# Kernel optimization log

Measured on AMD Instinct MI355X. Metric: run time of the kernel, lower is better.

## Reference

```python
import jax, jax.numpy as jnp
import numpy as np

N_PTS = 500000
R = 8            # channels per plane (num_channels=24 // 3)
FEAT = 24        # concat of 3 planes
HID = 168        # mlp_dim
OUT = 35
SIZES = [128, 256, 512]  # plane resolutions per level (plane_size=512, level_factor=0.5)
XYZ_MIN, XYZ_MAX = -2.0, 2.0


def setup_inputs() -> dict:
    key = jax.random.key(0)
    ks = jax.random.split(key, 64)
    inp = {"xyz": jax.random.uniform(ks[0], (N_PTS, 3), dtype=jnp.float32)}
    ki = 1
    for i, s in enumerate(SIZES):
        # planes stored [R, H, W]; torch init randn*0.1
        inp[f"xy{i}"] = jax.random.normal(ks[ki + 0], (R, s, s), dtype=jnp.float32) * 0.1
        inp[f"xz{i}"] = jax.random.normal(ks[ki + 1], (R, s, s), dtype=jnp.float32) * 0.1
        inp[f"yz{i}"] = jax.random.normal(ks[ki + 2], (R, s, s), dtype=jnp.float32) * 0.1
        inp[f"w1_{i}"] = jax.random.normal(ks[ki + 3], (FEAT, HID), dtype=jnp.float32) * 0.05
        inp[f"b1_{i}"] = jnp.zeros((HID,), jnp.float32)
        inp[f"w2_{i}"] = jax.random.normal(ks[ki + 4], (HID, HID), dtype=jnp.float32) * 0.05
        inp[f"b2_{i}"] = jnp.zeros((HID,), jnp.float32)
        inp[f"w3_{i}"] = jax.random.normal(ks[ki + 5], (HID, OUT), dtype=jnp.float32) * 0.05
        inp[f"b3_{i}"] = jnp.zeros((OUT,), jnp.float32)
        ki += 6
    return inp


def _bilinear(plane, gx, gy):
    # plane: [C,H,W]; gx in [-1,1] maps to W, gy maps to H; align_corners=True
    C, H, W = plane.shape
    ix = (gx + 1.0) * 0.5 * (W - 1)
    iy = (gy + 1.0) * 0.5 * (H - 1)
    x0 = jnp.floor(ix).astype(jnp.int32)
    y0 = jnp.floor(iy).astype(jnp.int32)
    wx = ix - x0
    wy = iy - y0
    x0c = jnp.clip(x0, 0, W - 1); x1c = jnp.clip(x0 + 1, 0, W - 1)
    y0c = jnp.clip(y0, 0, H - 1); y1c = jnp.clip(y0 + 1, 0, H - 1)
    v00 = plane[:, y0c, x0c]  # [C,N]
    v01 = plane[:, y0c, x1c]
    v10 = plane[:, y1c, x0c]
    v11 = plane[:, y1c, x1c]
    top = v00 * (1 - wx) + v01 * wx
    bot = v10 * (1 - wx) + v11 * wx
    return (top * (1 - wy) + bot * wy).T  # [N,C]


def _forward(xyz, planes, mlps):
    nrm = (xyz - XYZ_MIN) / (XYZ_MAX - XYZ_MIN) * 2.0 - 1.0  # [N,3]
    nx, ny, nz = nrm[:, 0], nrm[:, 1], nrm[:, 2]
    tmp = 0.0
    for (xy, xz, yz), (w1, b1, w2, b2, w3, b3) in zip(planes, mlps):
        # xy_plane[H=X,W=Y] sampled with grid (gx=ny, gy=nx), etc.
        feat = jnp.concatenate([
            _bilinear(xy, ny, nx),
            _bilinear(xz, nz, nx),
            _bilinear(yz, nz, ny),
        ], axis=-1)  # [N,24]
        h = jax.nn.relu(feat @ w1 + b1)
        h = jax.nn.relu(h @ w2 + b2)
        tmp = tmp + (h @ w3 + b3)
    # inference head: features[:27], rotations[27:31] raw; scale sigmoid; opacity*10
    return jnp.concatenate([tmp[:, :31], jax.nn.sigmoid(tmp[:, 31:34]), tmp[:, 34:] * 10.0], axis=-1)


def reference(xyz, xy0, xz0, yz0, w1_0, b1_0, w2_0, b2_0, w3_0, b3_0,
              xy1, xz1, yz1, w1_1, b1_1, w2_1, b2_1, w3_1, b3_1,
              xy2, xz2, yz2, w1_2, b1_2, w2_2, b2_2, w3_2, b3_2):
    planes = [(xy0, xz0, yz0), (xy1, xz1, yz1), (xy2, xz2, yz2)]
    mlps = [(w1_0, b1_0, w2_0, b2_0, w3_0, b3_0),
            (w1_1, b1_1, w2_1, b2_1, w3_1, b3_1),
            (w1_2, b1_2, w2_2, b2_2, w3_2, b3_2)]
    return _forward(xyz, planes, mlps)
```

## Files before the change

### kernel.cpp

```cpp
#include <hip/hip_runtime.h>

#define N_PTS 500000
#define FEAT 24
#define HID 168
#define OUT_C 35
#define MT 64
#define H_STR 176
#define WREG (32 * H_STR + 16)

#define WF1_OFF 0
#define WF2_OFF 18432
#define WF3_OFF 129024
#define W_TOTAL 156672
#define PL_S0 (W_TOTAL)
#define PL_S1 (PL_S0 + 393216)
#define PL_S2 (PL_S1 + 1572864)

#define PREP_W_BLOCKS 612

typedef short bf16x8 __attribute__((ext_vector_type(8)));
typedef float f32x4 __attribute__((ext_vector_type(4)));

__device__ __forceinline__ unsigned short f2bf(float f) {
    union { float f; unsigned int u; } v; v.f = f;
    unsigned int u = v.u;
    return (unsigned short)((u + 0x7FFFu + ((u >> 16) & 1u)) >> 16);
}
__device__ __forceinline__ float bf2f(unsigned short h) {
    union { unsigned int u; float f; } v; v.u = ((unsigned int)h) << 16;
    return v.f;
}
__device__ __forceinline__ unsigned int pk_bf16(float a, float b) {
    unsigned int r;
    asm("v_cvt_pk_bf16_f32 %0, %1, %2" : "=v"(r) : "v"(a), "v"(b));
    return r;
}
__device__ __forceinline__ f32x4 mfma16(bf16x8 a, bf16x8 b, f32x4 c) {
    return __builtin_amdgcn_mfma_f32_16x16x32_bf16(a, b, c, 0, 0, 0);
}

__global__ __launch_bounds__(256) void prep_all(
    const float* __restrict__ xy0, const float* __restrict__ xz0, const float* __restrict__ yz0,
    const float* __restrict__ xy1, const float* __restrict__ xz1, const float* __restrict__ yz1,
    const float* __restrict__ xy2, const float* __restrict__ xz2, const float* __restrict__ yz2,
    const float* __restrict__ w1a, const float* __restrict__ w2a, const float* __restrict__ w3a,
    const float* __restrict__ w1b, const float* __restrict__ w2b, const float* __restrict__ w3b,
    const float* __restrict__ w1c, const float* __restrict__ w2c, const float* __restrict__ w3c,
    const float* __restrict__ b1a, const float* __restrict__ b2a, const float* __restrict__ b3a,
    const float* __restrict__ b1b, const float* __restrict__ b2b, const float* __restrict__ b3b,
    const float* __restrict__ b1c, const float* __restrict__ b2c, const float* __restrict__ b3c,
    unsigned short* __restrict__ ws)
{
    if (blockIdx.x < PREP_W_BLOCKS) {
        int id = blockIdx.x * 256 + threadIdx.x;
        const float* w1[3] = {w1a, w1b, w1c};
        const float* w2[3] = {w2a, w2b, w2c};
        const float* w3[3] = {w3a, w3b, w3c};
        const float* b1[3] = {b1a, b1b, b1c};
        const float* b2[3] = {b2a, b2b, b2c};
        const float* b3[3] = {b3a, b3b, b3c};
        float v = 0.f;
        if (id < WF2_OFF) {
            int s = id / 6144, r = id % 6144;
            int mt = r >> 9, q = r & 511, lane = q >> 3, j = q & 7;
            int n = mt * 16 + (lane & 15), k = (lane >> 4) * 8 + j;
            if (n < HID) {
                if (k < FEAT)       v = w1[s][k * HID + n];
                else if (k == FEAT) v = b1[s][n];
            }
        } else if (id < WF3_OFF) {
            int t = id - WF2_OFF;
            int s = t / 36864, r = t % 36864;
            int fi = r >> 9, q = r & 511, lane = q >> 3, j = q & 7;
            int kk = fi / 12, mt = fi % 12;
            int n = mt * 16 + (lane & 15), k = kk * 32 + (lane >> 4) * 8 + j;
            if (n < HID) {
                if (k < HID)        v = w2[s][k * HID + n];
                else if (k == HID)  v = b2[s][n];
            }
        } else {
            int t = id - WF3_OFF;
            int s = t / 9216, r = t % 9216;
            int fi = r >> 9, q = r & 511, lane = q >> 3, j = q & 7;
            int mt = fi / 6, kk = fi % 6;
            int n = mt * 16 + (lane & 15), k = kk * 32 + (lane >> 4) * 8 + j;
            if (n < OUT_C) {
                if (k < HID)        v = w3[s][k * OUT_C + n];
                else if (k == HID)  v = b3[s][n];
            }
        }
        ws[id] = f2bf(v);
        return;
    }

    const float* pls[9] = {xy0, xz0, yz0, xy1, xz1, yz1, xy2, xz2, yz2};
    int b = blockIdx.x - PREP_W_BLOCKS;
    int s, pl, chunk, SS, base;
    if (b < 192)        { s = 0; SS = 16384;  pl = b / 64;   chunk = b % 64;    base = PL_S0; }
    else if (b < 960)   { int t = b - 192; s = 1; SS = 65536;  pl = t / 256;  chunk = t % 256;  base = PL_S1; }
    else                { int t = b - 960; s = 2; SS = 262144; pl = t / 1024; chunk = t % 1024; base = PL_S2; }
    const float* src = pls[s * 3 + pl];
    int pos = chunk * 256 + threadIdx.x;
    uint4 pk;
    unsigned int* po = (unsigned int*)&pk;
    #pragma unroll
    for (int c = 0; c < 4; ++c) {
        float f0 = src[(2 * c)     * SS + pos];
        float f1 = src[(2 * c + 1) * SS + pos];
        po[c] = pk_bf16(f0, f1);
    }
    *reinterpret_cast<uint4*>(&ws[base + pl * SS * 8 + pos * 8]) = pk;
}

__global__ __launch_bounds__(128, 4) void tri_mlp(
    const float* __restrict__ xyz,
    const unsigned short* __restrict__ wpack,
    float* __restrict__ out)
{
    __shared__ __align__(16) unsigned short H[2 * WREG];

    const int tid  = threadIdx.x;
    const int wave = tid >> 6;
    const int lane = tid & 63;
    const int quad = lane >> 4;
    const int l16  = lane & 15;
    const int p0   = blockIdx.x * MT;
    const int prow = wave * 32;
    unsigned short* Hw = H + wave * WREG;

    if (lane < 32)
        *reinterpret_cast<uint4*>(&Hw[lane * H_STR + HID]) = make_uint4(0x3F80u, 0u, 0u, 0u);
    if (lane < 8) ((unsigned int*)(Hw + 32 * H_STR))[lane] = 0u;

    float X[2], Y[2], Z[2];
    #pragma unroll
    for (int ni = 0; ni < 2; ++ni) {
        int gp = min(p0 + prow + ni * 16 + l16, N_PTS - 1);
        X[ni] = xyz[gp * 3 + 0];
        Y[ni] = xyz[gp * 3 + 1];
        Z[ni] = xyz[gp * 3 + 2];
    }

    f32x4 c3[2][3];
    #pragma unroll
    for (int mt = 0; mt < 3; ++mt) {
        c3[0][mt] = (f32x4){0.f, 0.f, 0.f, 0.f};
        c3[1][mt] = (f32x4){0.f, 0.f, 0.f, 0.f};
    }

    #pragma unroll 1
    for (int s = 0; s < 3; ++s) {
        int S, sbase;
        if (s == 0)      { S = 128; sbase = PL_S0; }
        else if (s == 1) { S = 256; sbase = PL_S1; }
        else             { S = 512; sbase = PL_S2; }

        bf16x8 B1[2];
        #pragma unroll
        for (int ni = 0; ni < 2; ++ni) {
            uint4 pk = {0x3F80u, 0u, 0u, 0u};
            if (quad < 3) {
                float gx, gy;
                if (quad == 0)      { gx = Y[ni]; gy = X[ni]; }
                else if (quad == 1) { gx = Z[ni]; gy = X[ni]; }
                else                { gx = Z[ni]; gy = Y[ni]; }
                gx *= 0.5f; gy *= 0.5f;
                float ix = (gx + 1.0f) * 0.5f * (float)(S - 1);
                float iy = (gy + 1.0f) * 0.5f * (float)(S - 1);
                float fx = floorf(ix), fy = floorf(iy);
                int x0 = (int)fx, y0 = (int)fy;
                float wx = ix - fx, wy = iy - fy;
                int x0c = min(max(x0, 0), S - 1);
                int x1c = min(x0 + 1, S - 1);
                int y0c = min(max(y0, 0), S - 1);
                int y1c = min(y0 + 1, S - 1);
                const unsigned short* pcl = wpack + sbase + (quad << 3) * S * S;
                uint4 q00 = *(const uint4*)&pcl[(y0c * S + x0c) * 8];
                uint4 q01 = *(const uint4*)&pcl[(y0c * S + x1c) * 8];
                uint4 q10 = *(const uint4*)&pcl[(y1c * S + x0c) * 8];
                uint4 q11 = *(const uint4*)&pcl[(y1c * S + x1c) * 8];
                float w00 = (1.f - wx) * (1.f - wy), w01 = wx * (1.f - wy);
                float w10 = (1.f - wx) * wy,         w11 = wx * wy;
                const unsigned int* u00 = (const unsigned int*)&q00;
                const unsigned int* u01 = (const unsigned int*)&q01;
                const unsigned int* u10 = (const unsigned int*)&q10;
                const unsigned int* u11 = (const unsigned int*)&q11;
                unsigned int* po = (unsigned int*)&pk;
                #pragma unroll
                for (int h = 0; h < 4; ++h) {
                    float a0 = bf2f((unsigned short)(u00[h] & 0xFFFF)) * w00
                             + bf2f((unsigned short)(u01[h] & 0xFFFF)) * w01
                             + bf2f((unsigned short)(u10[h] & 0xFFFF)) * w10
                             + bf2f((unsigned short)(u11[h] & 0xFFFF)) * w11;
                    float a1 = bf2f((unsigned short)(u00[h] >> 16)) * w00
                             + bf2f((unsigned short)(u01[h] >> 16)) * w01
                             + bf2f((unsigned short)(u10[h] >> 16)) * w10
                             + bf2f((unsigned short)(u11[h] >> 16)) * w11;
                    po[h] = pk_bf16(a0, a1);
                }
            }
            B1[ni] = *reinterpret_cast<bf16x8*>(&pk);
        }

        {
            const unsigned short* w1f = wpack + WF1_OFF + s * 6144;
            #pragma unroll
            for (int mt = 0; mt < 11; ++mt) {
                bf16x8 a = *(const bf16x8*)&w1f[mt * 512 + lane * 8];
                #pragma unroll
                for (int ni = 0; ni < 2; ++ni) {
                    f32x4 c = mfma16(a, B1[ni], (f32x4){0.f, 0.f, 0.f, 0.f});
                    unsigned int u0 = pk_bf16(fmaxf(c[0], 0.f), fmaxf(c[1], 0.f));
                    unsigned int u1 = pk_bf16(fmaxf(c[2], 0.f), fmaxf(c[3], 0.f));
                    if (mt < 10 || quad < 2)
                        *reinterpret_cast<uint2*>(&Hw[(ni * 16 + l16) * H_STR + mt * 16 + quad * 4]) =
                            make_uint2(u0, u1);
                }
            }
        }

        bf16x8 B2[2][6];
        #pragma unroll
        for (int ni = 0; ni < 2; ++ni)
            #pragma unroll
            for (int kk = 0; kk < 6; ++kk)
                B2[ni][kk] = *(const bf16x8*)&Hw[(ni * 16 + l16) * H_STR + kk * 32 + quad * 8];

        {
            const unsigned short* w2f = wpack + WF2_OFF + s * 36864;
            #pragma unroll 1
            for (int mt = 0; mt < 11; ++mt) {
                f32x4 c20 = {0.f, 0.f, 0.f, 0.f};
                f32x4 c21 = c20;
                #pragma unroll
                for (int kk = 0; kk < 6; ++kk) {
                    bf16x8 a = *(const bf16x8*)&w2f[(kk * 12 + mt) * 512 + lane * 8];
                    c20 = mfma16(a, B2[0][kk], c20);
                    c21 = mfma16(a, B2[1][kk], c21);
                }
                if (mt < 10 || quad < 2) {
                    unsigned int u00 = pk_bf16(fmaxf(c20[0], 0.f), fmaxf(c20[1], 0.f));
                    unsigned int u01 = pk_bf16(fmaxf(c20[2], 0.f), fmaxf(c20[3], 0.f));
                    *reinterpret_cast<uint2*>(&Hw[(l16) * H_STR + mt * 16 + quad * 4]) =
                        make_uint2(u00, u01);
                    unsigned int u10 = pk_bf16(fmaxf(c21[0], 0.f), fmaxf(c21[1], 0.f));
                    unsigned int u11 = pk_bf16(fmaxf(c21[2], 0.f), fmaxf(c21[3], 0.f));
                    *reinterpret_cast<uint2*>(&Hw[(16 + l16) * H_STR + mt * 16 + quad * 4]) =
                        make_uint2(u10, u11);
                }
            }
        }

        {
            const unsigned short* w3f = wpack + WF3_OFF + s * 9216;
            #pragma unroll 1
            for (int kk = 0; kk < 6; ++kk) {
                bf16x8 b30 = *(const bf16x8*)&Hw[(l16) * H_STR + kk * 32 + quad * 8];
                bf16x8 b31 = *(const bf16x8*)&Hw[(16 + l16) * H_STR + kk * 32 + quad * 8];
                #pragma unroll
                for (int mt = 0; mt < 3; ++mt) {
                    bf16x8 a = *(const bf16x8*)&w3f[(mt * 6 + kk) * 512 + lane * 8];
                    c3[0][mt] = mfma16(a, b30, c3[0][mt]);
                    c3[1][mt] = mfma16(a, b31, c3[1][mt]);
                }
            }
        }
    }

    float* Hf = (float*)Hw;
    #pragma unroll
    for (int ni = 0; ni < 2; ++ni) {
        int row = ni * 16 + l16;
        #pragma unroll
        for (int mt = 0; mt < 3; ++mt) {
            #pragma unroll
            for (int r = 0; r < 4; ++r) {
                int ch = mt * 16 + quad * 4 + r;
                if (ch < OUT_C) {
                    float v = c3[ni][mt][r];
                    if (ch >= 31 && ch < 34)      v = 1.0f / (1.0f + expf(-v));
                    else if (ch == 34)            v *= 10.0f;
                    Hf[row * 35 + ch] = v;
                }
            }
        }
    }
    if (p0 + prow < N_PTS) {
        const int base = (p0 + prow) * 35;
        #pragma unroll
        for (int t = 0; t < 5; ++t) {
            int off = t * 256 + lane * 4;
            if (off < 1120) {
                f32x4 v = *(const f32x4*)&Hf[off];
                __builtin_nontemporal_store(v, reinterpret_cast<f32x4*>(&out[base + off]));
            }
        }
    }
}

extern "C" void kernel_launch(void* const* d_in, const int* in_sizes, int n_in,
                              void* d_out, int out_size, void* d_ws, size_t ws_size,
                              hipStream_t stream) {
    (void)in_sizes; (void)n_in; (void)out_size; (void)ws_size;
    const float* xyz  = (const float*)d_in[0];
    const float* xy0  = (const float*)d_in[1];
    const float* xz0  = (const float*)d_in[2];
    const float* yz0  = (const float*)d_in[3];
    const float* w1_0 = (const float*)d_in[4];
    const float* b1_0 = (const float*)d_in[5];
    const float* w2_0 = (const float*)d_in[6];
    const float* b2_0 = (const float*)d_in[7];
    const float* w3_0 = (const float*)d_in[8];
    const float* b3_0 = (const float*)d_in[9];
    const float* xy1  = (const float*)d_in[10];
    const float* xz1  = (const float*)d_in[11];
    const float* yz1  = (const float*)d_in[12];
    const float* w1_1 = (const float*)d_in[13];
    const float* b1_1 = (const float*)d_in[14];
    const float* w2_1 = (const float*)d_in[15];
    const float* b2_1 = (const float*)d_in[16];
    const float* w3_1 = (const float*)d_in[17];
    const float* b3_1 = (const float*)d_in[18];
    const float* xy2  = (const float*)d_in[19];
    const float* xz2  = (const float*)d_in[20];
    const float* yz2  = (const float*)d_in[21];
    const float* w1_2 = (const float*)d_in[22];
    const float* b1_2 = (const float*)d_in[23];
    const float* w2_2 = (const float*)d_in[24];
    const float* b2_2 = (const float*)d_in[25];
    const float* w3_2 = (const float*)d_in[26];
    const float* b3_2 = (const float*)d_in[27];

    unsigned short* ws = (unsigned short*)d_ws;
    float* out = (float*)d_out;

    prep_all<<<PREP_W_BLOCKS + 4032, 256, 0, stream>>>(
        xy0, xz0, yz0, xy1, xz1, yz1, xy2, xz2, yz2,
        w1_0, w2_0, w3_0, w1_1, w2_1, w3_1, w1_2, w2_2, w3_2,
        b1_0, b2_0, b3_0, b1_1, b2_1, b3_1, b1_2, b2_2, b3_2,
        ws);

    tri_mlp<<<(N_PTS + MT - 1) / MT, 128, 0, stream>>>(xyz, ws, out);
}
```

Baseline: 351.6 us.

## Halve points per wave to 16 and raise occupancy target

Each wave now handles one 16-point MFMA column tile instead of two, so the block tile drops from 64 to 32 points and the per-wave LDS region shrinks. Launch bounds go from 4 to 6 blocks per SM, aiming for more resident waves to hide the latency of the bilinear gathers. The trade-off is that each weight fragment loaded from global/L2 now feeds only one MFMA instead of two, which doubles weight traffic per point. The bounds clamp was removed because 500000 is divisible by 32.

```diff
diff --git a/kernel.cpp b/kernel.cpp
--- a/kernel.cpp
+++ b/kernel.cpp
@@ -4,9 +4,9 @@
 #define FEAT 24
 #define HID 168
 #define OUT_C 35
-#define MT 64
+#define MT 32
 #define H_STR 176
-#define WREG (32 * H_STR + 16)
+#define WREG (16 * H_STR + 16)
 
 #define WF1_OFF 0
 #define WF2_OFF 18432
@@ -112,7 +112,7 @@
     *reinterpret_cast<uint4*>(&ws[base + pl * SS * 8 + pos * 8]) = pk;
 }
 
-__global__ __launch_bounds__(128, 4) void tri_mlp(
+__global__ __launch_bounds__(128, 6) void tri_mlp(
     const float* __restrict__ xyz,
     const unsigned short* __restrict__ wpack,
     float* __restrict__ out)
@@ -125,28 +125,21 @@
     const int quad = lane >> 4;
     const int l16  = lane & 15;
     const int p0   = blockIdx.x * MT;
-    const int prow = wave * 32;
+    const int prow = wave * 16;
     unsigned short* Hw = H + wave * WREG;
 
-    if (lane < 32)
+    if (lane < 16)
         *reinterpret_cast<uint4*>(&Hw[lane * H_STR + HID]) = make_uint4(0x3F80u, 0u, 0u, 0u);
-    if (lane < 8) ((unsigned int*)(Hw + 32 * H_STR))[lane] = 0u;
-
-    float X[2], Y[2], Z[2];
+    if (lane < 8) ((unsigned int*)(Hw + 16 * H_STR))[lane] = 0u;
+
+    const int gp = p0 + prow + l16;
+    const float X = xyz[gp * 3 + 0];
+    const float Y = xyz[gp * 3 + 1];
+    const float Z = xyz[gp * 3 + 2];
+
+    f32x4 c3[3];
     #pragma unroll
-    for (int ni = 0; ni < 2; ++ni) {
-        int gp = min(p0 + prow + ni * 16 + l16, N_PTS - 1);
-        X[ni] = xyz[gp * 3 + 0];
-        Y[ni] = xyz[gp * 3 + 1];
-        Z[ni] = xyz[gp * 3 + 2];
-    }
-
-    f32x4 c3[2][3];
-    #pragma unroll
-    for (int mt = 0; mt < 3; ++mt) {
-        c3[0][mt] = (f32x4){0.f, 0.f, 0.f, 0.f};
-        c3[1][mt] = (f32x4){0.f, 0.f, 0.f, 0.f};
-    }
+    for (int mt = 0; mt < 3; ++mt) c3[mt] = (f32x4){0.f, 0.f, 0.f, 0.f};
 
     #pragma unroll 1
     for (int s = 0; s < 3; ++s) {
@@ -155,15 +148,14 @@
         else if (s == 1) { S = 256; sbase = PL_S1; }
         else             { S = 512; sbase = PL_S2; }
 
-        bf16x8 B1[2];
-        #pragma unroll
-        for (int ni = 0; ni < 2; ++ni) {
+        bf16x8 B1;
+        {
             uint4 pk = {0x3F80u, 0u, 0u, 0u};
             if (quad < 3) {
                 float gx, gy;
-                if (quad == 0)      { gx = Y[ni]; gy = X[ni]; }
-                else if (quad == 1) { gx = Z[ni]; gy = X[ni]; }
-                else                { gx = Z[ni]; gy = Y[ni]; }
+                if (quad == 0)      { gx = Y; gy = X; }
+                else if (quad == 1) { gx = Z; gy = X; }
+                else                { gx = Z; gy = Y; }
                 gx *= 0.5f; gy *= 0.5f;
                 float ix = (gx + 1.0f) * 0.5f * (float)(S - 1);
                 float iy = (gy + 1.0f) * 0.5f * (float)(S - 1);
@@ -199,7 +191,7 @@
                     po[h] = pk_bf16(a0, a1);
                 }
             }
-            B1[ni] = *reinterpret_cast<bf16x8*>(&pk);
+            B1 = *reinterpret_cast<bf16x8*>(&pk);
         }
 
         {
@@ -207,46 +199,35 @@
             #pragma unroll
             for (int mt = 0; mt < 11; ++mt) {
                 bf16x8 a = *(const bf16x8*)&w1f[mt * 512 + lane * 8];
-                #pragma unroll
-                for (int ni = 0; ni < 2; ++ni) {
-                    f32x4 c = mfma16(a, B1[ni], (f32x4){0.f, 0.f, 0.f, 0.f});
-                    unsigned int u0 = pk_bf16(fmaxf(c[0], 0.f), fmaxf(c[1], 0.f));
-                    unsigned int u1 = pk_bf16(fmaxf(c[2], 0.f), fmaxf(c[3], 0.f));
-                    if (mt < 10 || quad < 2)
-                        *reinterpret_cast<uint2*>(&Hw[(ni * 16 + l16) * H_STR + mt * 16 + quad * 4]) =
-                            make_uint2(u0, u1);
-                }
-            }
-        }
-
-        bf16x8 B2[2][6];
+                f32x4 c = mfma16(a, B1, (f32x4){0.f, 0.f, 0.f, 0.f});
+                unsigned int u0 = pk_bf16(fmaxf(c[0], 0.f), fmaxf(c[1], 0.f));
+                unsigned int u1 = pk_bf16(fmaxf(c[2], 0.f), fmaxf(c[3], 0.f));
+                if (mt < 10 || quad < 2)
+                    *reinterpret_cast<uint2*>(&Hw[l16 * H_STR + mt * 16 + quad * 4]) =
+                        make_uint2(u0, u1);
+            }
+        }
+
+        bf16x8 B2[6];
         #pragma unroll
-        for (int ni = 0; ni < 2; ++ni)
-            #pragma unroll
-            for (int kk = 0; kk < 6; ++kk)
-                B2[ni][kk] = *(const bf16x8*)&Hw[(ni * 16 + l16) * H_STR + kk * 32 + quad * 8];
+        for (int kk = 0; kk < 6; ++kk)
+            B2[kk] = *(const bf16x8*)&Hw[l16 * H_STR + kk * 32 + quad * 8];
 
         {
             const unsigned short* w2f = wpack + WF2_OFF + s * 36864;
             #pragma unroll 1
             for (int mt = 0; mt < 11; ++mt) {
-                f32x4 c20 = {0.f, 0.f, 0.f, 0.f};
-                f32x4 c21 = c20;
+                f32x4 c2 = {0.f, 0.f, 0.f, 0.f};
                 #pragma unroll
                 for (int kk = 0; kk < 6; ++kk) {
                     bf16x8 a = *(const bf16x8*)&w2f[(kk * 12 + mt) * 512 + lane * 8];
-                    c20 = mfma16(a, B2[0][kk], c20);
-                    c21 = mfma16(a, B2[1][kk], c21);
+                    c2 = mfma16(a, B2[kk], c2);
                 }
                 if (mt < 10 || quad < 2) {
-                    unsigned int u00 = pk_bf16(fmaxf(c20[0], 0.f), fmaxf(c20[1], 0.f));
-                    unsigned int u01 = pk_bf16(fmaxf(c20[2], 0.f), fmaxf(c20[3], 0.f));
-                    *reinterpret_cast<uint2*>(&Hw[(l16) * H_STR + mt * 16 + quad * 4]) =
-                        make_uint2(u00, u01);
-                    unsigned int u10 = pk_bf16(fmaxf(c21[0], 0.f), fmaxf(c21[1], 0.f));
-                    unsigned int u11 = pk_bf16(fmaxf(c21[2], 0.f), fmaxf(c21[3], 0.f));
-                    *reinterpret_cast<uint2*>(&Hw[(16 + l16) * H_STR + mt * 16 + quad * 4]) =
-                        make_uint2(u10, u11);
+                    unsigned int u0 = pk_bf16(fmaxf(c2[0], 0.f), fmaxf(c2[1], 0.f));
+                    unsigned int u1 = pk_bf16(fmaxf(c2[2], 0.f), fmaxf(c2[3], 0.f));
+                    *reinterpret_cast<uint2*>(&Hw[l16 * H_STR + mt * 16 + quad * 4]) =
+                        make_uint2(u0, u1);
                 }
             }
         }
@@ -255,29 +236,26 @@
             const unsigned short* w3f = wpack + WF3_OFF + s * 9216;
             #pragma unroll 1
             for (int kk = 0; kk < 6; ++kk) {
-                bf16x8 b30 = *(const bf16x8*)&Hw[(l16) * H_STR + kk * 32 + quad * 8];
-                bf16x8 b31 = *(const bf16x8*)&Hw[(16 + l16) * H_STR + kk * 32 + quad * 8];
+                bf16x8 b3 = *(const bf16x8*)&Hw[l16 * H_STR + kk * 32 + quad * 8];
                 #pragma unroll
                 for (int mt = 0; mt < 3; ++mt) {
                     bf16x8 a = *(const bf16x8*)&w3f[(mt * 6 + kk) * 512 + lane * 8];
-                    c3[0][mt] = mfma16(a, b30, c3[0][mt]);
-                    c3[1][mt] = mfma16(a, b31, c3[1][mt]);
+                    c3[mt] = mfma16(a, b3, c3[mt]);
                 }
             }
         }
     }
 
     float* Hf = (float*)Hw;
-    #pragma unroll
-    for (int ni = 0; ni < 2; ++ni) {
-        int row = ni * 16 + l16;
+    {
+        int row = l16;
         #pragma unroll
         for (int mt = 0; mt < 3; ++mt) {
             #pragma unroll
             for (int r = 0; r < 4; ++r) {
                 int ch = mt * 16 + quad * 4 + r;
                 if (ch < OUT_C) {
-                    float v = c3[ni][mt][r];
+                    float v = c3[mt][r];
                     if (ch >= 31 && ch < 34)      v = 1.0f / (1.0f + expf(-v));
                     else if (ch == 34)            v *= 10.0f;
                     Hf[row * 35 + ch] = v;
@@ -285,12 +263,12 @@
             }
         }
     }
-    if (p0 + prow < N_PTS) {
+    {
         const int base = (p0 + prow) * 35;
         #pragma unroll
-        for (int t = 0; t < 5; ++t) {
+        for (int t = 0; t < 3; ++t) {
             int off = t * 256 + lane * 4;
-            if (off < 1120) {
+            if (off < 560) {
                 f32x4 v = *(const f32x4*)&Hf[off];
                 __builtin_nontemporal_store(v, reinterpret_cast<f32x4*>(&out[base + off]));
             }
```

Result: slower. 449.7 us (+27.9%).

## Prefetch next level's bilinear corner loads before current level's MLP

Applied to the files above, without the earlier changes.

Splits the plane sampling into an issue phase, which computes indices and loads the four corner vectors, and a consume phase, which does the weighting and packing. The next level's corner gathers are issued right after the current level's features are packed, so their latency can overlap the MLP MFMA work. The first level's loads are issued before the LDS initialisation. This holds 16 extra uint4 values in registers, which may raise register pressure and lower occupancy under launch_bounds(128,4).

```diff
diff --git a/kernel.cpp b/kernel.cpp
--- a/kernel.cpp
+++ b/kernel.cpp
@@ -128,10 +128,6 @@
     const int prow = wave * 32;
     unsigned short* Hw = H + wave * WREG;
 
-    if (lane < 32)
-        *reinterpret_cast<uint4*>(&Hw[lane * H_STR + HID]) = make_uint4(0x3F80u, 0u, 0u, 0u);
-    if (lane < 8) ((unsigned int*)(Hw + 32 * H_STR))[lane] = 0u;
-
     float X[2], Y[2], Z[2];
     #pragma unroll
     for (int ni = 0; ni < 2; ++ni) {
@@ -141,6 +137,37 @@
         Z[ni] = xyz[gp * 3 + 2];
     }
 
+    uint4 Q[2][4];
+    auto issue_corners = [&](int S, int sbase) {
+        if (quad < 3) {
+            #pragma unroll
+            for (int ni = 0; ni < 2; ++ni) {
+                float gx, gy;
+                if (quad == 0)      { gx = Y[ni]; gy = X[ni]; }
+                else if (quad == 1) { gx = Z[ni]; gy = X[ni]; }
+                else                { gx = Z[ni]; gy = Y[ni]; }
+                float ix = (gx * 0.5f + 1.0f) * 0.5f * (float)(S - 1);
+                float iy = (gy * 0.5f + 1.0f) * 0.5f * (float)(S - 1);
+                int x0 = (int)floorf(ix), y0 = (int)floorf(iy);
+                int x0c = min(max(x0, 0), S - 1);
+                int x1c = min(x0 + 1, S - 1);
+                int y0c = min(max(y0, 0), S - 1);
+                int y1c = min(y0 + 1, S - 1);
+                const unsigned short* pcl = wpack + sbase + (quad << 3) * S * S;
+                Q[ni][0] = *(const uint4*)&pcl[(y0c * S + x0c) * 8];
+                Q[ni][1] = *(const uint4*)&pcl[(y0c * S + x1c) * 8];
+                Q[ni][2] = *(const uint4*)&pcl[(y1c * S + x0c) * 8];
+                Q[ni][3] = *(const uint4*)&pcl[(y1c * S + x1c) * 8];
+            }
+        }
+    };
+
+    issue_corners(128, PL_S0);
+
+    if (lane < 32)
+        *reinterpret_cast<uint4*>(&Hw[lane * H_STR + HID]) = make_uint4(0x3F80u, 0u, 0u, 0u);
+    if (lane < 8) ((unsigned int*)(Hw + 32 * H_STR))[lane] = 0u;
+
     f32x4 c3[2][3];
     #pragma unroll
     for (int mt = 0; mt < 3; ++mt) {
@@ -150,10 +177,7 @@
 
     #pragma unroll 1
     for (int s = 0; s < 3; ++s) {
-        int S, sbase;
-        if (s == 0)      { S = 128; sbase = PL_S0; }
-        else if (s == 1) { S = 256; sbase = PL_S1; }
-        else             { S = 512; sbase = PL_S2; }
+        const int S = (s == 0) ? 128 : (s == 1) ? 256 : 512;
 
         bf16x8 B1[2];
         #pragma unroll
@@ -164,27 +188,15 @@
                 if (quad == 0)      { gx = Y[ni]; gy = X[ni]; }
                 else if (quad == 1) { gx = Z[ni]; gy = X[ni]; }
                 else                { gx = Z[ni]; gy = Y[ni]; }
-                gx *= 0.5f; gy *= 0.5f;
-                float ix = (gx + 1.0f) * 0.5f * (float)(S - 1);
-                float iy = (gy + 1.0f) * 0.5f * (float)(S - 1);
-                float fx = floorf(ix), fy = floorf(iy);
-                int x0 = (int)fx, y0 = (int)fy;
-                float wx = ix - fx, wy = iy - fy;
-                int x0c = min(max(x0, 0), S - 1);
-                int x1c = min(x0 + 1, S - 1);
-                int y0c = min(max(y0, 0), S - 1);
-                int y1c = min(y0 + 1, S - 1);
-                const unsigned short* pcl = wpack + sbase + (quad << 3) * S * S;
-                uint4 q00 = *(const uint4*)&pcl[(y0c * S + x0c) * 8];
-                uint4 q01 = *(const uint4*)&pcl[(y0c * S + x1c) * 8];
-                uint4 q10 = *(const uint4*)&pcl[(y1c * S + x0c) * 8];
-                uint4 q11 = *(const uint4*)&pcl[(y1c * S + x1c) * 8];
+                float ix = (gx * 0.5f + 1.0f) * 0.5f * (float)(S - 1);
+                float iy = (gy * 0.5f + 1.0f) * 0.5f * (float)(S - 1);
+                float wx = ix - floorf(ix), wy = iy - floorf(iy);
                 float w00 = (1.f - wx) * (1.f - wy), w01 = wx * (1.f - wy);
                 float w10 = (1.f - wx) * wy,         w11 = wx * wy;
-                const unsigned int* u00 = (const unsigned int*)&q00;
-                const unsigned int* u01 = (const unsigned int*)&q01;
-                const unsigned int* u10 = (const unsigned int*)&q10;
-                const unsigned int* u11 = (const unsigned int*)&q11;
+                const unsigned int* u00 = (const unsigned int*)&Q[ni][0];
+                const unsigned int* u01 = (const unsigned int*)&Q[ni][1];
+                const unsigned int* u10 = (const unsigned int*)&Q[ni][2];
+                const unsigned int* u11 = (const unsigned int*)&Q[ni][3];
                 unsigned int* po = (unsigned int*)&pk;
                 #pragma unroll
                 for (int h = 0; h < 4; ++h) {
@@ -201,6 +213,9 @@
             }
             B1[ni] = *reinterpret_cast<bf16x8*>(&pk);
         }
+
+        if (s == 0)      issue_corners(256, PL_S1);
+        else if (s == 1) issue_corners(512, PL_S2);
 
         {
             const unsigned short* w1f = wpack + WF1_OFF + s * 6144;
```

After: 478.2 us. 36.0% more time.
